# Kernel tuning notes

Measured on AMD Instinct MI355X. Metric: run time of the kernel, lower is better.

Reference implementation:

```python
import jax, jax.numpy as jnp
import numpy as np

M, L, D, V = 4096, 15, 1024, 32  # moves, word_max, in_sz, vocab_sz


def setup_inputs() -> dict:
    key = jax.random.key(0)
    ks = jax.random.split(key, 9)
    s = 0.02
    return {
        "tokens": jax.random.randint(ks[0], (M, L), 0, V),
        "letter_emb": jax.random.normal(ks[1], (V, D), jnp.float32) * s,
        "pos_emb": jax.random.normal(ks[2], (L, D), jnp.float32) * s,
        "Wq": jax.random.normal(ks[3], (D, D), jnp.float32) * s,
        "bq": jax.random.normal(ks[4], (D,), jnp.float32) * s,
        "Wk": jax.random.normal(ks[5], (D, D), jnp.float32) * s,
        "bk": jax.random.normal(ks[6], (D,), jnp.float32) * s,
        "Wv": jax.random.normal(ks[7], (D, D), jnp.float32) * s,
        "bv": jax.random.normal(ks[8], (D,), jnp.float32) * s,
    }


def reference(tokens, letter_emb, pos_emb, Wq, bq, Wk, bk, Wv, bv):
    # WordEncoder, batched across all M moves.
    x = letter_emb[tokens] + pos_emb[None, :, :]          # [M, L, D]
    q = jnp.einsum("mld,ed->mle", x, Wq) + bq             # Linear: x @ W.T + b
    k = jnp.einsum("mld,ed->mle", x, Wk) + bk
    v = jnp.einsum("mld,ed->mle", x, Wv) + bv
    scores = jax.nn.softmax(jnp.einsum("mle,mke->mlk", q, k), axis=-1)  # [M, L, L]
    attn = jnp.einsum("mlk,mke->mle", scores, v)          # [M, L, D]
    word = attn.sum(axis=1)                               # [M, D]
    # enc = word + ordered, where ordered is an identical second evaluation
    # of word_enc on the same word -> enc = 2 * word.
    return 2.0 * word
```

## Files before the change

### kernel.cpp

```cpp
#include <hip/hip_runtime.h>
#include <hip/hip_bf16.h>

#define NMOVES 4096
#define LW     15
#define DIM    1024
#define VOC    32
#define NROW   480
#define XROW   48
#define G48LD  64

typedef __attribute__((ext_vector_type(8))) short  short8;
typedef __attribute__((ext_vector_type(4))) float  floatx4;

__device__ __forceinline__ unsigned short f2b(float f) {
  unsigned int x;
  __builtin_memcpy(&x, &f, 4);
  x = x + 0x7FFFu + ((x >> 16) & 1u);
  return (unsigned short)(x >> 16);
}
__device__ __forceinline__ ushort4 cvt4(float4 v) {
  ushort4 o; o.x = f2b(v.x); o.y = f2b(v.y); o.z = f2b(v.z); o.w = f2b(v.w);
  return o;
}
__device__ __forceinline__ float b2f(unsigned short u) {
  unsigned int x = ((unsigned int)u) << 16;
  float f;
  __builtin_memcpy(&f, &x, 4);
  return f;
}

#define LDK 72

__global__ __launch_bounds__(256) void proj_small(
    const float* __restrict__ letter, const float* __restrict__ pos,
    const float* __restrict__ Wq, const float* __restrict__ Wk,
    const float* __restrict__ Wv,
    float* __restrict__ Xq, float* __restrict__ Xk, float* __restrict__ Xv) {
  __shared__ __attribute__((aligned(16))) unsigned short lA[64 * LDK];
  __shared__ __attribute__((aligned(16))) unsigned short lB[64 * LDK];

  const float* W = (blockIdx.z == 0) ? Wq : (blockIdx.z == 1) ? Wk : Wv;
  float*       O = (blockIdx.z == 0) ? Xq : (blockIdx.z == 1) ? Xk : Xv;

  const int bn0 = blockIdx.y * 64;

  const int tid  = threadIdx.x;
  const int lane = tid & 63;
  const int wave = tid >> 6;
  const int wr   = wave >> 1;
  const int wc   = wave & 1;
  const int quad = lane >> 4;
  const int l16  = lane & 15;
  const int srow = tid >> 3;
  const int scol = (tid & 7) << 3;

  const float* aptr0 = letter + (size_t)srow * DIM + scol;
  const bool   av1   = (srow < LW);
  const float* aptr1 = av1 ? (pos + (size_t)srow * DIM + scol) : letter;
  const float* bptr0 = W + (size_t)(bn0 + srow) * DIM + scol;
  const float* bptr1 = bptr0 + (size_t)32 * DIM;

  const float4 z4 = make_float4(0.f, 0.f, 0.f, 0.f);
  float4 ra00 = *reinterpret_cast<const float4*>(aptr0);
  float4 ra01 = *reinterpret_cast<const float4*>(aptr0 + 4);
  float4 ra10 = av1 ? *reinterpret_cast<const float4*>(aptr1)     : z4;
  float4 ra11 = av1 ? *reinterpret_cast<const float4*>(aptr1 + 4) : z4;
  float4 rb00 = *reinterpret_cast<const float4*>(bptr0);
  float4 rb01 = *reinterpret_cast<const float4*>(bptr0 + 4);
  float4 rb10 = *reinterpret_cast<const float4*>(bptr1);
  float4 rb11 = *reinterpret_cast<const float4*>(bptr1 + 4);

  floatx4 acc[2][2];
#pragma unroll
  for (int i = 0; i < 2; ++i)
#pragma unroll
    for (int j = 0; j < 2; ++j) acc[i][j] = (floatx4){0.f, 0.f, 0.f, 0.f};

  for (int k0 = 0; k0 < DIM; k0 += 64) {
    *reinterpret_cast<ushort4*>(lA + srow * LDK + scol)            = cvt4(ra00);
    *reinterpret_cast<ushort4*>(lA + srow * LDK + scol + 4)        = cvt4(ra01);
    *reinterpret_cast<ushort4*>(lA + (srow + 32) * LDK + scol)     = cvt4(ra10);
    *reinterpret_cast<ushort4*>(lA + (srow + 32) * LDK + scol + 4) = cvt4(ra11);
    *reinterpret_cast<ushort4*>(lB + srow * LDK + scol)            = cvt4(rb00);
    *reinterpret_cast<ushort4*>(lB + srow * LDK + scol + 4)        = cvt4(rb01);
    *reinterpret_cast<ushort4*>(lB + (srow + 32) * LDK + scol)     = cvt4(rb10);
    *reinterpret_cast<ushort4*>(lB + (srow + 32) * LDK + scol + 4) = cvt4(rb11);
    __syncthreads();
    if (k0 + 64 < DIM) {
      const int k = k0 + 64;
      ra00 = *reinterpret_cast<const float4*>(aptr0 + k);
      ra01 = *reinterpret_cast<const float4*>(aptr0 + k + 4);
      ra10 = av1 ? *reinterpret_cast<const float4*>(aptr1 + k)     : z4;
      ra11 = av1 ? *reinterpret_cast<const float4*>(aptr1 + k + 4) : z4;
      rb00 = *reinterpret_cast<const float4*>(bptr0 + k);
      rb01 = *reinterpret_cast<const float4*>(bptr0 + k + 4);
      rb10 = *reinterpret_cast<const float4*>(bptr1 + k);
      rb11 = *reinterpret_cast<const float4*>(bptr1 + k + 4);
    }
#pragma unroll
    for (int kk = 0; kk < 64; kk += 32) {
      short8 a0 = *reinterpret_cast<const short8*>(lA + (wr * 32 + l16) * LDK + kk + quad * 8);
      short8 a1 = *reinterpret_cast<const short8*>(lA + (wr * 32 + 16 + l16) * LDK + kk + quad * 8);
      short8 b0 = *reinterpret_cast<const short8*>(lB + (wc * 32 + l16) * LDK + kk + quad * 8);
      short8 b1 = *reinterpret_cast<const short8*>(lB + (wc * 32 + 16 + l16) * LDK + kk + quad * 8);
      acc[0][0] = __builtin_amdgcn_mfma_f32_16x16x32_bf16(a0, b0, acc[0][0], 0, 0, 0);
      acc[0][1] = __builtin_amdgcn_mfma_f32_16x16x32_bf16(a0, b1, acc[0][1], 0, 0, 0);
      acc[1][0] = __builtin_amdgcn_mfma_f32_16x16x32_bf16(a1, b0, acc[1][0], 0, 0, 0);
      acc[1][1] = __builtin_amdgcn_mfma_f32_16x16x32_bf16(a1, b1, acc[1][1], 0, 0, 0);
    }
    __syncthreads();
  }

#pragma unroll
  for (int mi = 0; mi < 2; ++mi) {
#pragma unroll
    for (int ni = 0; ni < 2; ++ni) {
      const int gcol = bn0 + wc * 32 + ni * 16 + l16;
#pragma unroll
      for (int i = 0; i < 4; ++i) {
        const int grow = wr * 32 + mi * 16 + quad * 4 + i;
        if (grow < XROW - 1)
          O[(size_t)grow * DIM + gcol] = acc[mi][ni][i];
      }
    }
  }
}

__global__ __launch_bounds__(256) void gram_vexp(
    const float* __restrict__ Xq, const float* __restrict__ Xk,
    const float* __restrict__ bq, const float* __restrict__ bk,
    const float* __restrict__ Xv, const float* __restrict__ bv,
    float* __restrict__ G48, unsigned short* __restrict__ Vb) {
  const int tid = threadIdx.x;

  if (blockIdx.x == 0) {
    __shared__ __attribute__((aligned(16))) unsigned short lA[64 * LDK];
    __shared__ __attribute__((aligned(16))) unsigned short lB[64 * LDK];

    const int lane = tid & 63;
    const int wave = tid >> 6;
    const int wr   = wave >> 1;
    const int wc   = wave & 1;
    const int quad = lane >> 4;
    const int l16  = lane & 15;
    const int srow = tid >> 3;
    const int scol = (tid & 7) << 3;

    const float* aptr0 = Xq + (size_t)srow * DIM + scol;
    const float* bptr0 = Xk + (size_t)srow * DIM + scol;
    const bool   v1    = (srow <= LW);
    const float* aptr1 = (srow < LW) ? (Xq + (size_t)(32 + srow) * DIM + scol)
                                     : (srow == LW ? (bq + scol) : Xq);
    const float* bptr1 = (srow < LW) ? (Xk + (size_t)(32 + srow) * DIM + scol)
                                     : (srow == LW ? (bk + scol) : Xk);

    const float4 z4 = make_float4(0.f, 0.f, 0.f, 0.f);
    float4 ra00 = *reinterpret_cast<const float4*>(aptr0);
    float4 ra01 = *reinterpret_cast<const float4*>(aptr0 + 4);
    float4 ra10 = v1 ? *reinterpret_cast<const float4*>(aptr1)     : z4;
    float4 ra11 = v1 ? *reinterpret_cast<const float4*>(aptr1 + 4) : z4;
    float4 rb00 = *reinterpret_cast<const float4*>(bptr0);
    float4 rb01 = *reinterpret_cast<const float4*>(bptr0 + 4);
    float4 rb10 = v1 ? *reinterpret_cast<const float4*>(bptr1)     : z4;
    float4 rb11 = v1 ? *reinterpret_cast<const float4*>(bptr1 + 4) : z4;

    floatx4 acc[2][2];
#pragma unroll
    for (int i = 0; i < 2; ++i)
#pragma unroll
      for (int j = 0; j < 2; ++j) acc[i][j] = (floatx4){0.f, 0.f, 0.f, 0.f};

    for (int k0 = 0; k0 < DIM; k0 += 64) {
      *reinterpret_cast<ushort4*>(lA + srow * LDK + scol)            = cvt4(ra00);
      *reinterpret_cast<ushort4*>(lA + srow * LDK + scol + 4)        = cvt4(ra01);
      *reinterpret_cast<ushort4*>(lA + (srow + 32) * LDK + scol)     = cvt4(ra10);
      *reinterpret_cast<ushort4*>(lA + (srow + 32) * LDK + scol + 4) = cvt4(ra11);
      *reinterpret_cast<ushort4*>(lB + srow * LDK + scol)            = cvt4(rb00);
      *reinterpret_cast<ushort4*>(lB + srow * LDK + scol + 4)        = cvt4(rb01);
      *reinterpret_cast<ushort4*>(lB + (srow + 32) * LDK + scol)     = cvt4(rb10);
      *reinterpret_cast<ushort4*>(lB + (srow + 32) * LDK + scol + 4) = cvt4(rb11);
      __syncthreads();
      if (k0 + 64 < DIM) {
        const int k = k0 + 64;
        ra00 = *reinterpret_cast<const float4*>(aptr0 + k);
        ra01 = *reinterpret_cast<const float4*>(aptr0 + k + 4);
        ra10 = v1 ? *reinterpret_cast<const float4*>(aptr1 + k)     : z4;
        ra11 = v1 ? *reinterpret_cast<const float4*>(aptr1 + k + 4) : z4;
        rb00 = *reinterpret_cast<const float4*>(bptr0 + k);
        rb01 = *reinterpret_cast<const float4*>(bptr0 + k + 4);
        rb10 = v1 ? *reinterpret_cast<const float4*>(bptr1 + k)     : z4;
        rb11 = v1 ? *reinterpret_cast<const float4*>(bptr1 + k + 4) : z4;
      }
#pragma unroll
      for (int kk = 0; kk < 64; kk += 32) {
        short8 a0 = *reinterpret_cast<const short8*>(lA + (wr * 32 + l16) * LDK + kk + quad * 8);
        short8 a1 = *reinterpret_cast<const short8*>(lA + (wr * 32 + 16 + l16) * LDK + kk + quad * 8);
        short8 b0 = *reinterpret_cast<const short8*>(lB + (wc * 32 + l16) * LDK + kk + quad * 8);
        short8 b1 = *reinterpret_cast<const short8*>(lB + (wc * 32 + 16 + l16) * LDK + kk + quad * 8);
        acc[0][0] = __builtin_amdgcn_mfma_f32_16x16x32_bf16(a0, b0, acc[0][0], 0, 0, 0);
        acc[0][1] = __builtin_amdgcn_mfma_f32_16x16x32_bf16(a0, b1, acc[0][1], 0, 0, 0);
        acc[1][0] = __builtin_amdgcn_mfma_f32_16x16x32_bf16(a1, b0, acc[1][0], 0, 0, 0);
        acc[1][1] = __builtin_amdgcn_mfma_f32_16x16x32_bf16(a1, b1, acc[1][1], 0, 0, 0);
      }
      __syncthreads();
    }

#pragma unroll
    for (int mi = 0; mi < 2; ++mi) {
#pragma unroll
      for (int ni = 0; ni < 2; ++ni) {
        const int gcol = wc * 32 + ni * 16 + l16;
#pragma unroll
        for (int i = 0; i < 4; ++i) {
          const int grow = wr * 32 + mi * 16 + quad * 4 + i;
          if (grow < XROW)
            G48[(size_t)grow * G48LD + gcol] = acc[mi][ni][i];
        }
      }
    }
  } else {
    const int c   = (blockIdx.x - 1) * 256 + tid;
    const int row = c >> 7;
    const int col = (c & 127) << 3;
    const int t   = row / LW;
    const int l   = row - t * LW;
    const float* lv = Xv + (size_t)t * DIM + col;
    const float* pv = Xv + (size_t)(32 + l) * DIM + col;
    const float* bb = bv + col;
    float4 x0 = *reinterpret_cast<const float4*>(lv);
    float4 x1 = *reinterpret_cast<const float4*>(lv + 4);
    float4 p0 = *reinterpret_cast<const float4*>(pv);
    float4 p1 = *reinterpret_cast<const float4*>(pv + 4);
    float4 b0 = *reinterpret_cast<const float4*>(bb);
    float4 b1 = *reinterpret_cast<const float4*>(bb + 4);
    ushort4 o0, o1;
    o0.x = f2b(x0.x + p0.x + b0.x); o0.y = f2b(x0.y + p0.y + b0.y);
    o0.z = f2b(x0.z + p0.z + b0.z); o0.w = f2b(x0.w + p0.w + b0.w);
    o1.x = f2b(x1.x + p1.x + b1.x); o1.y = f2b(x1.y + p1.y + b1.y);
    o1.z = f2b(x1.z + p1.z + b1.z); o1.w = f2b(x1.w + p1.w + b1.w);
    *reinterpret_cast<ushort4*>(Vb + (size_t)row * DIM + col)     = o0;
    *reinterpret_cast<ushort4*>(Vb + (size_t)row * DIM + col + 4) = o1;
  }
}

__global__ __launch_bounds__(256) void attn_out_k(
    const void* __restrict__ tokens_raw, const float* __restrict__ G48,
    const unsigned short* __restrict__ Vb, float* __restrict__ out) {
  __shared__ __attribute__((aligned(16))) float Gs[XROW * G48LD];
  __shared__ int   tok[LW];
  __shared__ int   ridx[LW];
  __shared__ float S[LW][16];
  __shared__ float w[16];
  __shared__ int   is64_s;
  const int m = blockIdx.x;
  const int tid = threadIdx.x;

  const unsigned int* u32 = (const unsigned int*)tokens_raw;
  if (tid < 64) {
    unsigned int v = u32[2 * tid + 1];
    unsigned long long nz = __ballot(v != 0);
    if (tid == 0) is64_s = (nz == 0ULL) ? 1 : 0;
  }
  __syncthreads();

  if (tid < LW) {
    int t;
    if (is64_s) t = (int)((const long long*)tokens_raw)[m * LW + tid];
    else        t = ((const int*)tokens_raw)[m * LW + tid];
    tok[tid]  = t;
    ridx[tid] = t * LW + tid;
  }
#pragma unroll
  for (int i = 0; i < 3; ++i) {
    const int idx = i * 256 + tid;
    reinterpret_cast<float4*>(Gs)[idx] =
        reinterpret_cast<const float4*>(G48)[idx];
  }
  __syncthreads();

  if (tid < LW * LW) {
    const int l = tid / LW;
    const int j = tid - l * LW;
    const int a0 = tok[l], a1 = 32 + l;
    const int b0 = tok[j], b1 = 32 + j;
    S[l][j] = Gs[a0 * G48LD + b0] + Gs[a0 * G48LD + b1] +
              Gs[a1 * G48LD + b0] + Gs[a1 * G48LD + b1] +
              Gs[(XROW - 1) * G48LD + b0] + Gs[(XROW - 1) * G48LD + b1];
  }
  __syncthreads();

  if (tid < LW) {
    float mx = -1e30f;
#pragma unroll
    for (int j = 0; j < LW; ++j) mx = fmaxf(mx, S[tid][j]);
    float s = 0.f;
#pragma unroll
    for (int j = 0; j < LW; ++j) { float e = __expf(S[tid][j] - mx); S[tid][j] = e; s += e; }
    const float inv = 1.0f / s;
#pragma unroll
    for (int j = 0; j < LW; ++j) S[tid][j] *= inv;
  }
  __syncthreads();

  if (tid < LW) {
    float s = 0.f;
#pragma unroll
    for (int l = 0; l < LW; ++l) s += S[l][tid];
    w[tid] = 2.0f * s;
  }
  __syncthreads();

  const int e0 = tid * 4;
  float a0 = 0.f, a1 = 0.f, a2 = 0.f, a3 = 0.f;
#pragma unroll
  for (int j = 0; j < LW; ++j) {
    const float wj = w[j];
    ushort4 vv = *reinterpret_cast<const ushort4*>(Vb + (size_t)ridx[j] * DIM + e0);
    a0 += wj * b2f(vv.x);
    a1 += wj * b2f(vv.y);
    a2 += wj * b2f(vv.z);
    a3 += wj * b2f(vv.w);
  }
  *reinterpret_cast<float4*>(out + (size_t)m * DIM + e0) =
      make_float4(a0, a1, a2, a3);
}

extern "C" void kernel_launch(void* const* d_in, const int* in_sizes, int n_in,
                              void* d_out, int out_size, void* d_ws, size_t ws_size,
                              hipStream_t stream) {
  const void*  tokens = d_in[0];
  const float* letter = (const float*)d_in[1];
  const float* pos    = (const float*)d_in[2];
  const float* Wq     = (const float*)d_in[3];
  const float* bq     = (const float*)d_in[4];
  const float* Wk     = (const float*)d_in[5];
  const float* bk     = (const float*)d_in[6];
  const float* Wv     = (const float*)d_in[7];
  const float* bv     = (const float*)d_in[8];
  float*       outp   = (float*)d_out;

  char* ws = (char*)d_ws;
  const size_t XSZ  = (size_t)XROW * DIM * 4;
  const size_t GSZ  = (size_t)G48LD * G48LD * 4;
  float* Xq = (float*)(ws);
  float* Xk = (float*)(ws + XSZ);
  float* Xv = (float*)(ws + 2 * XSZ);
  float* Gp = (float*)(ws + 3 * XSZ);
  unsigned short* Vb = (unsigned short*)(ws + 3 * XSZ + GSZ);

  proj_small<<<dim3(1, 16, 3), 256, 0, stream>>>(letter, pos, Wq, Wk, Wv,
                                                 Xq, Xk, Xv);
  gram_vexp<<<1 + (NROW * DIM / 8 / 256), 256, 0, stream>>>(Xq, Xk, bq, bk,
                                                            Xv, bv, Gp, Vb);
  attn_out_k<<<NMOVES, 256, 0, stream>>>(tokens, Gp, Vb, outp);
}
```

Measured before the change: 137.5 us.

## Replace per-move gather with coefficient vector times projected-V GEMM

The output stage is reformulated so each move's output is a 48-entry weight vector over the letter, position and bias rows, multiplied by a transposed bf16 copy of the projected V. A new coefficient kernel handles 16 moves per block, and an MFMA GEMM computes the outputs with a hi/lo bf16 split of the coefficients. The V-bias term is added as a constant of 30 times bv. This drops the expanded 480-row V table and the per-move gathers, at the cost of an extra kernel launch and a split-precision GEMM.

New measurement: 136.7 us. Within noise of the previous version (-0.5%).

```diff
diff --git a/kernel.cpp b/kernel.cpp
--- a/kernel.cpp
+++ b/kernel.cpp
@@ -129,8 +129,8 @@
 __global__ __launch_bounds__(256) void gram_vexp(
     const float* __restrict__ Xq, const float* __restrict__ Xk,
     const float* __restrict__ bq, const float* __restrict__ bk,
-    const float* __restrict__ Xv, const float* __restrict__ bv,
-    float* __restrict__ G48, unsigned short* __restrict__ Vb) {
+    const float* __restrict__ Xv,
+    float* __restrict__ G48, unsigned short* __restrict__ XvT) {
   const int tid = threadIdx.x;
 
   if (blockIdx.x == 0) {
@@ -219,40 +219,29 @@
       }
     }
   } else {
-    const int c   = (blockIdx.x - 1) * 256 + tid;
-    const int row = c >> 7;
-    const int col = (c & 127) << 3;
-    const int t   = row / LW;
-    const int l   = row - t * LW;
-    const float* lv = Xv + (size_t)t * DIM + col;
-    const float* pv = Xv + (size_t)(32 + l) * DIM + col;
-    const float* bb = bv + col;
-    float4 x0 = *reinterpret_cast<const float4*>(lv);
-    float4 x1 = *reinterpret_cast<const float4*>(lv + 4);
-    float4 p0 = *reinterpret_cast<const float4*>(pv);
-    float4 p1 = *reinterpret_cast<const float4*>(pv + 4);
-    float4 b0 = *reinterpret_cast<const float4*>(bb);
-    float4 b1 = *reinterpret_cast<const float4*>(bb + 4);
-    ushort4 o0, o1;
-    o0.x = f2b(x0.x + p0.x + b0.x); o0.y = f2b(x0.y + p0.y + b0.y);
-    o0.z = f2b(x0.z + p0.z + b0.z); o0.w = f2b(x0.w + p0.w + b0.w);
-    o1.x = f2b(x1.x + p1.x + b1.x); o1.y = f2b(x1.y + p1.y + b1.y);
-    o1.z = f2b(x1.z + p1.z + b1.z); o1.w = f2b(x1.w + p1.w + b1.w);
-    *reinterpret_cast<ushort4*>(Vb + (size_t)row * DIM + col)     = o0;
-    *reinterpret_cast<ushort4*>(Vb + (size_t)row * DIM + col + 4) = o1;
-  }
-}
-
-__global__ __launch_bounds__(256) void attn_out_k(
+    const int n  = ((int)blockIdx.x - 1) * 16 + (tid >> 4);
+    const int k0 = (tid & 15) * 4;
+    float v[4];
+#pragma unroll
+    for (int i = 0; i < 4; ++i) {
+      const int k = k0 + i;
+      v[i] = (k < XROW - 1) ? Xv[(size_t)k * DIM + n] : 0.f;
+    }
+    ushort4 o;
+    o.x = f2b(v[0]); o.y = f2b(v[1]); o.z = f2b(v[2]); o.w = f2b(v[3]);
+    *reinterpret_cast<ushort4*>(XvT + (size_t)n * 64 + k0) = o;
+  }
+}
+
+__global__ __launch_bounds__(256) void coef_k(
     const void* __restrict__ tokens_raw, const float* __restrict__ G48,
-    const unsigned short* __restrict__ Vb, float* __restrict__ out) {
-  __shared__ __attribute__((aligned(16))) float Gs[XROW * G48LD];
-  __shared__ int   tok[LW];
-  __shared__ int   ridx[LW];
-  __shared__ float S[LW][16];
-  __shared__ float w[16];
+    unsigned short* __restrict__ C) {
+  __shared__ float Gs[XROW * 65];
+  __shared__ float Sm[16][LW][17];
+  __shared__ float CL[16][64];
+  __shared__ int   tokL[16][16];
   __shared__ int   is64_s;
-  const int m = blockIdx.x;
+  const int m0  = blockIdx.x * 16;
   const int tid = threadIdx.x;
 
   const unsigned int* u32 = (const unsigned int*)tokens_raw;
@@ -261,68 +250,128 @@
     unsigned long long nz = __ballot(v != 0);
     if (tid == 0) is64_s = (nz == 0ULL) ? 1 : 0;
   }
+#pragma unroll
+  for (int i = 0; i < 12; ++i) {
+    const int idx = i * 256 + tid;
+    Gs[(idx >> 6) * 65 + (idx & 63)] = G48[idx];
+  }
+  {
+    const int g = tid >> 4, L = tid & 15;
+#pragma unroll
+    for (int i = 0; i < 4; ++i) CL[g][L * 4 + i] = 0.f;
+  }
   __syncthreads();
 
-  if (tid < LW) {
+  if (tid < 16 * LW) {
+    const int mv = tid / LW, j = tid - mv * LW;
     int t;
-    if (is64_s) t = (int)((const long long*)tokens_raw)[m * LW + tid];
-    else        t = ((const int*)tokens_raw)[m * LW + tid];
-    tok[tid]  = t;
-    ridx[tid] = t * LW + tid;
-  }
-#pragma unroll
-  for (int i = 0; i < 3; ++i) {
-    const int idx = i * 256 + tid;
-    reinterpret_cast<float4*>(Gs)[idx] =
-        reinterpret_cast<const float4*>(G48)[idx];
+    if (is64_s) t = (int)((const long long*)tokens_raw)[(size_t)(m0 + mv) * LW + j];
+    else        t = ((const int*)tokens_raw)[(size_t)(m0 + mv) * LW + j];
+    tokL[mv][j] = t;
   }
   __syncthreads();
 
-  if (tid < LW * LW) {
-    const int l = tid / LW;
-    const int j = tid - l * LW;
-    const int a0 = tok[l], a1 = 32 + l;
-    const int b0 = tok[j], b1 = 32 + j;
-    S[l][j] = Gs[a0 * G48LD + b0] + Gs[a0 * G48LD + b1] +
-              Gs[a1 * G48LD + b0] + Gs[a1 * G48LD + b1] +
-              Gs[(XROW - 1) * G48LD + b0] + Gs[(XROW - 1) * G48LD + b1];
+  const int g = tid >> 4;
+  const int L = tid & 15;
+  if (L < LW) {
+    const int rb0 = tokL[g][L] * 65;
+    const int rb1 = (32 + L) * 65;
+    const int rb2 = (XROW - 1) * 65;
+    float S[LW];
+#pragma unroll
+    for (int j = 0; j < LW; ++j) {
+      const int c0 = tokL[g][j];
+      const int c1 = 32 + j;
+      S[j] = Gs[rb0 + c0] + Gs[rb1 + c0] + Gs[rb2 + c0]
+           + Gs[rb0 + c1] + Gs[rb1 + c1] + Gs[rb2 + c1];
+    }
+    float mx = S[0];
+#pragma unroll
+    for (int j = 1; j < LW; ++j) mx = fmaxf(mx, S[j]);
+    float sum = 0.f;
+#pragma unroll
+    for (int j = 0; j < LW; ++j) { S[j] = __expf(S[j] - mx); sum += S[j]; }
+    const float inv = 1.0f / sum;
+#pragma unroll
+    for (int j = 0; j < LW; ++j) Sm[g][L][j] = S[j] * inv;
   }
   __syncthreads();
 
-  if (tid < LW) {
-    float mx = -1e30f;
-#pragma unroll
-    for (int j = 0; j < LW; ++j) mx = fmaxf(mx, S[tid][j]);
+  if (L < LW) {
     float s = 0.f;
 #pragma unroll
-    for (int j = 0; j < LW; ++j) { float e = __expf(S[tid][j] - mx); S[tid][j] = e; s += e; }
-    const float inv = 1.0f / s;
-#pragma unroll
-    for (int j = 0; j < LW; ++j) S[tid][j] *= inv;
+    for (int l = 0; l < LW; ++l) s += Sm[g][l][L];
+    const float wj = 2.0f * s;
+    atomicAdd(&CL[g][tokL[g][L]], wj);
+    CL[g][32 + L] = wj;
   }
   __syncthreads();
 
-  if (tid < LW) {
-    float s = 0.f;
-#pragma unroll
-    for (int l = 0; l < LW; ++l) s += S[l][tid];
-    w[tid] = 2.0f * s;
-  }
-  __syncthreads();
-
-  const int e0 = tid * 4;
-  float a0 = 0.f, a1 = 0.f, a2 = 0.f, a3 = 0.f;
-#pragma unroll
-  for (int j = 0; j < LW; ++j) {
-    const float wj = w[j];
-    ushort4 vv = *reinterpret_cast<const ushort4*>(Vb + (size_t)ridx[j] * DIM + e0);
-    a0 += wj * b2f(vv.x);
-    a1 += wj * b2f(vv.y);
-    a2 += wj * b2f(vv.z);
-    a3 += wj * b2f(vv.w);
-  }
-  *reinterpret_cast<float4*>(out + (size_t)m * DIM + e0) =
-      make_float4(a0, a1, a2, a3);
+  float4 cv = *reinterpret_cast<const float4*>(&CL[g][L * 4]);
+  ushort4 hi, lo;
+  hi.x = f2b(cv.x); hi.y = f2b(cv.y); hi.z = f2b(cv.z); hi.w = f2b(cv.w);
+  lo.x = f2b(cv.x - b2f(hi.x)); lo.y = f2b(cv.y - b2f(hi.y));
+  lo.z = f2b(cv.z - b2f(hi.z)); lo.w = f2b(cv.w - b2f(hi.w));
+  unsigned short* Crow = C + (size_t)(m0 + g) * 128;
+  *reinterpret_cast<ushort4*>(Crow + L * 4)      = hi;
+  *reinterpret_cast<ushort4*>(Crow + 64 + L * 4) = lo;
+}
+
+__global__ __launch_bounds__(256) void out_gemm(
+    const unsigned short* __restrict__ C, const unsigned short* __restrict__ XvT,
+    const float* __restrict__ bv, float* __restrict__ out) {
+  const int bm0 = blockIdx.x * 64;
+  const int bn0 = blockIdx.y * 64;
+  const int tid  = threadIdx.x;
+  const int lane = tid & 63;
+  const int wave = tid >> 6;
+  const int wr   = wave >> 1;
+  const int wc   = wave & 1;
+  const int quad = lane >> 4;
+  const int l16  = lane & 15;
+
+  const unsigned short* A0 = C + (size_t)(bm0 + wr * 32 + l16) * 128;
+  const unsigned short* A1 = A0 + 16 * 128;
+  const unsigned short* B0 = XvT + (size_t)(bn0 + wc * 32 + l16) * 64;
+  const unsigned short* B1 = B0 + 16 * 64;
+
+  floatx4 acc[2][2];
+#pragma unroll
+  for (int i = 0; i < 2; ++i)
+#pragma unroll
+    for (int j = 0; j < 2; ++j) acc[i][j] = (floatx4){0.f, 0.f, 0.f, 0.f};
+
+#pragma unroll
+  for (int ks = 0; ks < 64; ks += 32) {
+    short8 b0  = *reinterpret_cast<const short8*>(B0 + ks + quad * 8);
+    short8 b1  = *reinterpret_cast<const short8*>(B1 + ks + quad * 8);
+    short8 a0h = *reinterpret_cast<const short8*>(A0 + ks + quad * 8);
+    short8 a1h = *reinterpret_cast<const short8*>(A1 + ks + quad * 8);
+    short8 a0l = *reinterpret_cast<const short8*>(A0 + 64 + ks + quad * 8);
+    short8 a1l = *reinterpret_cast<const short8*>(A1 + 64 + ks + quad * 8);
+    acc[0][0] = __builtin_amdgcn_mfma_f32_16x16x32_bf16(a0h, b0, acc[0][0], 0, 0, 0);
+    acc[0][0] = __builtin_amdgcn_mfma_f32_16x16x32_bf16(a0l, b0, acc[0][0], 0, 0, 0);
+    acc[0][1] = __builtin_amdgcn_mfma_f32_16x16x32_bf16(a0h, b1, acc[0][1], 0, 0, 0);
+    acc[0][1] = __builtin_amdgcn_mfma_f32_16x16x32_bf16(a0l, b1, acc[0][1], 0, 0, 0);
+    acc[1][0] = __builtin_amdgcn_mfma_f32_16x16x32_bf16(a1h, b0, acc[1][0], 0, 0, 0);
+    acc[1][0] = __builtin_amdgcn_mfma_f32_16x16x32_bf16(a1l, b0, acc[1][0], 0, 0, 0);
+    acc[1][1] = __builtin_amdgcn_mfma_f32_16x16x32_bf16(a1h, b1, acc[1][1], 0, 0, 0);
+    acc[1][1] = __builtin_amdgcn_mfma_f32_16x16x32_bf16(a1l, b1, acc[1][1], 0, 0, 0);
+  }
+
+#pragma unroll
+  for (int mi = 0; mi < 2; ++mi) {
+#pragma unroll
+    for (int ni = 0; ni < 2; ++ni) {
+      const int gcol = bn0 + wc * 32 + ni * 16 + l16;
+      const float bias30 = 30.0f * bv[gcol];
+#pragma unroll
+      for (int i = 0; i < 4; ++i) {
+        const int grow = bm0 + wr * 32 + mi * 16 + quad * 4 + i;
+        out[(size_t)grow * DIM + gcol] = acc[mi][ni][i] + bias30;
+      }
+    }
+  }
 }
 
 extern "C" void kernel_launch(void* const* d_in, const int* in_sizes, int n_in,
@@ -341,16 +390,18 @@
 
   char* ws = (char*)d_ws;
   const size_t XSZ  = (size_t)XROW * DIM * 4;
-  const size_t GSZ  = (size_t)G48LD * G48LD * 4;
+  const size_t GSZ  = (size_t)XROW * G48LD * 4;
   float* Xq = (float*)(ws);
   float* Xk = (float*)(ws + XSZ);
   float* Xv = (float*)(ws + 2 * XSZ);
   float* Gp = (float*)(ws + 3 * XSZ);
-  unsigned short* Vb = (unsigned short*)(ws + 3 * XSZ + GSZ);
+  unsigned short* XvT = (unsigned short*)(ws + 3 * XSZ + 16384);
+  unsigned short* Cc  = (unsigned short*)(ws + 3 * XSZ + 16384 + (size_t)DIM * 64 * 2);
+  (void)GSZ;
 
   proj_small<<<dim3(1, 16, 3), 256, 0, stream>>>(letter, pos, Wq, Wk, Wv,
                                                  Xq, Xk, Xv);
-  gram_vexp<<<1 + (NROW * DIM / 8 / 256), 256, 0, stream>>>(Xq, Xk, bq, bk,
-                                                            Xv, bv, Gp, Vb);
-  attn_out_k<<<NMOVES, 256, 0, stream>>>(tokens, Gp, Vb, outp);
-}
+  gram_vexp<<<65, 256, 0, stream>>>(Xq, Xk, bq, bk, Xv, Gp, XvT);
+  coef_k<<<NMOVES / 16, 256, 0, stream>>>(tokens, Gp, Cc);
+  out_gemm<<<dim3(NMOVES / 64, DIM / 64), 256, 0, stream>>>(Cc, XvT, bv, outp);
+}
```
